# Performance work log

Measured on AMD Instinct MI355X. Metric: run time of the kernel, lower is better.

The kernel has to match this reference:

```python
import jax, jax.numpy as jnp
import numpy as np

N_STEPS = 8          # spatial_interval
SPATIAL_SCALE = 1.0  # spatial_scale


def setup_inputs() -> dict:
    key = jax.random.key(0)
    ks = jax.random.split(key, 6)
    B, N, D = 32, 1024, 256
    x = jax.random.normal(ks[0], (B, N, D), dtype=jnp.float32)
    adj_mx = jax.random.uniform(ks[1], (N, N), dtype=jnp.float32) / N  # row-scaled dense adjacency
    alpha_train = jnp.ones((N,), dtype=jnp.float32)          # alpha * ones(num_node), alpha=1.0
    w = jnp.eye(D, dtype=jnp.float32) + 0.01 * jax.random.normal(ks[2], (D, D), dtype=jnp.float32)
    d = jax.random.uniform(ks[3], (D,), dtype=jnp.float32)
    fc_in_w = jax.random.normal(ks[4], (D, D), dtype=jnp.float32) * (1.0 / np.sqrt(D))
    fc_in_b = jnp.zeros((D,), dtype=jnp.float32)
    return {"x": x, "adj_mx": adj_mx, "alpha_train": alpha_train, "w": w,
            "d": d, "fc_in_w": fc_in_w, "fc_in_b": fc_in_b, "vt": 0}


def reference(x, adj_mx, alpha_train, w, d, fc_in_w, fc_in_b, vt):
    # x: [B, N, D]. x0 is detached in torch (x.clone().detach()).
    x0 = jax.lax.stop_gradient(x)
    # fc_in (dropout is identity in eval mode)
    h = jnp.einsum('bnd,ed->bne', x, fc_in_w) + fc_in_b
    # constants of the diffusion ODE
    alph = jax.nn.sigmoid(alpha_train)[:, None]          # [N, 1]
    d_clamped = jnp.clip(d, 0.0, 1.0)
    w_eff = (w * d_clamped) @ w.T                        # [D, D]
    dt = jnp.float32(SPATIAL_SCALE / N_STEPS)

    def euler_step(h, _):
        ax = jnp.einsum('nm,bmd->bnd', adj_mx, h)        # graph diffusion
        f = alph * 0.5 * (ax - h) + h @ w_eff - h + x0
        return h + dt * f, None

    h, _ = jax.lax.scan(euler_step, h, None, length=N_STEPS)
    return h
```

## Files before the change

### kernel.cpp

```cpp
#include <hip/hip_runtime.h>
#include <hip/hip_bf16.h>
#include <stdint.h>

typedef __bf16 bf16;
typedef __bf16 bf16x8 __attribute__((ext_vector_type(8)));
typedef __bf16 bf16x4 __attribute__((ext_vector_type(4)));
typedef float f32x4 __attribute__((ext_vector_type(4)));

#define BM 128
#define BN 64
#define BK 64

__device__ __forceinline__ void gload_lds16(const bf16* g, bf16* l) {
    __builtin_amdgcn_global_load_lds(
        (const __attribute__((address_space(1))) void*)g,
        (__attribute__((address_space(3))) void*)l, 16, 0, 0);
}

template <int CH>
__device__ __forceinline__ void stageT(const bf16* __restrict__ g, int ld,
                                       bf16* l, int t) {
#pragma unroll
    for (int i = 0; i < CH / 256; ++i) {
        int c = (i << 8) + t;
        gload_lds16(g + (size_t)(c >> 3) * ld + ((c & 7) << 3), l + c * 8);
    }
}

__device__ __forceinline__ void mma_128x64(const bf16* As, const bf16* Bs,
                                           f32x4 acc[4][2], int lane, int wm, int wn) {
    const int rA = wm * 64 + (lane & 15);
    const int rB = wn * 32 + (lane & 15);
    const int kb = (lane >> 4) * 8;
#pragma unroll
    for (int kk = 0; kk < 2; ++kk) {
        bf16x8 a[4], b[2];
#pragma unroll
        for (int mi = 0; mi < 4; ++mi)
            a[mi] = *(const bf16x8*)&As[(rA + mi * 16) * BK + kk * 32 + kb];
#pragma unroll
        for (int ni = 0; ni < 2; ++ni)
            b[ni] = *(const bf16x8*)&Bs[(rB + ni * 16) * BK + kk * 32 + kb];
#pragma unroll
        for (int mi = 0; mi < 4; ++mi)
#pragma unroll
            for (int ni = 0; ni < 2; ++ni)
                acc[mi][ni] = __builtin_amdgcn_mfma_f32_16x16x32_bf16(
                    a[mi], b[ni], acc[mi][ni], 0, 0, 0);
    }
}

__global__ void prep_alpha(const float* __restrict__ a, float* __restrict__ out) {
    int i = blockIdx.x * blockDim.x + threadIdx.x;
    if (i < 1024) out[i] = 0.5f / (1.0f + __expf(-a[i]));
}

__global__ void prep_adj(const float* __restrict__ adj, const float* __restrict__ ahs,
                         bf16* __restrict__ adjb) {
    int i = blockIdx.x * blockDim.x + threadIdx.x;
    int row = i >> 8;
    float s = ahs[row];
    float4 v = ((const float4*)adj)[i];
    bf16x4 o = {(bf16)(s * v.x), (bf16)(s * v.y), (bf16)(s * v.z), (bf16)(s * v.w)};
    ((bf16x4*)adjb)[i] = o;
}

__global__ void cast_f32_bf16x4(const float* __restrict__ src, bf16* __restrict__ dst,
                                int n4) {
    int i = blockIdx.x * blockDim.x + threadIdx.x;
    if (i < n4) {
        float4 v = ((const float4*)src)[i];
        bf16x4 o = {(bf16)v.x, (bf16)v.y, (bf16)v.z, (bf16)v.w};
        ((bf16x4*)dst)[i] = o;
    }
}

__global__ void prep_weff(const float* __restrict__ w, const float* __restrict__ dv,
                          bf16* __restrict__ weffT) {
    __shared__ float wk[256];
    __shared__ float dd[256];
    int k = blockIdx.x, j = threadIdx.x;
    dd[j] = fminf(fmaxf(dv[j], 0.0f), 1.0f);
    wk[j] = w[k * 256 + j];
    __syncthreads();
    float s = 0.0f;
#pragma unroll 8
    for (int c = 0; c < 256; ++c) s += wk[c] * dd[c] * w[j * 256 + c];
    weffT[j * 256 + k] = (bf16)s;
}

__launch_bounds__(256)
__global__ void gemm_fcin(const bf16* __restrict__ xb, const bf16* __restrict__ fcwb,
                          const float* __restrict__ fcb, float* __restrict__ hf,
                          bf16* __restrict__ hb, bf16* __restrict__ hT) {
    __shared__ __align__(16) bf16 As[BM * BK];
    __shared__ __align__(16) bf16 Bs[BN * BK];
    int t = threadIdx.x, lane = t & 63, wv = t >> 6, wm = wv >> 1, wn = wv & 1;
    int row0 = blockIdx.y * BM;
    int col0 = blockIdx.x * BN;
    f32x4 acc[4][2] = {};
    const bf16* Ab = xb + (size_t)row0 * 256;
    const bf16* Bb = fcwb + (size_t)col0 * 256;
    for (int kt = 0; kt < 4; ++kt) {
        __syncthreads();
        stageT<1024>(Ab + kt * BK, 256, As, t);
        stageT<512>(Bb + kt * BK, 256, Bs, t);
        __syncthreads();
        mma_128x64(As, Bs, acc, lane, wm, wn);
    }
    int rbase = row0 + wm * 64 + ((lane >> 4) << 2);
    int cbase = col0 + wn * 32 + (lane & 15);
#pragma unroll
    for (int mi = 0; mi < 4; ++mi) {
        int rg = rbase + mi * 16;
#pragma unroll
        for (int ni = 0; ni < 2; ++ni) {
            int col = cbase + ni * 16;
            float bias = fcb[col];
            bf16x4 tv;
#pragma unroll
            for (int r = 0; r < 4; ++r) {
                float v = acc[mi][ni][r] + bias;
                size_t idx = (size_t)(rg + r) * 256 + col;
                hf[idx] = v;
                bf16 vb = (bf16)v;
                hb[idx] = vb;
                tv[r] = vb;
            }
            int b = rg >> 10, n = rg & 1023;
            *(bf16x4*)&hT[(((size_t)(b * 256 + col)) << 10) + n] = tv;
        }
    }
}

__launch_bounds__(256)
__global__ void gemm_step(const bf16* __restrict__ adjb, const bf16* __restrict__ hbp,
                          const bf16* __restrict__ hTp, const bf16* __restrict__ weffT,
                          const float* __restrict__ ahs, const bf16* __restrict__ x0b,
                          float* __restrict__ hf, bf16* __restrict__ hbn,
                          bf16* __restrict__ hTn) {
    __shared__ __align__(16) bf16 As[BM * BK];
    __shared__ __align__(16) bf16 Bs[BN * BK];
    int t = threadIdx.x, lane = t & 63, wv = t >> 6, wm = wv >> 1, wn = wv & 1;
    int g = blockIdx.x;
    int xcd = g & 7, rest = g >> 3;
    int xy = rest & 31, bhi = rest >> 5;
    int b = bhi * 8 + xcd;
    int d0 = (xy & 3) * BN;
    int n0 = (xy >> 2) * BM;
    f32x4 acc[4][2] = {};

    const bf16* Ab1 = adjb + (size_t)n0 * 1024;
    const bf16* Bb1 = hTp + ((size_t)(b * 256 + d0)) * 1024;
    for (int kt = 0; kt < 16; ++kt) {
        __syncthreads();
        stageT<1024>(Ab1 + kt * BK, 1024, As, t);
        stageT<512>(Bb1 + kt * BK, 1024, Bs, t);
        __syncthreads();
        mma_128x64(As, Bs, acc, lane, wm, wn);
    }
    const bf16* Ab2 = hbp + ((size_t)(b * 1024 + n0)) * 256;
    const bf16* Bb2 = weffT + (size_t)d0 * 256;
    for (int kt = 0; kt < 4; ++kt) {
        __syncthreads();
        stageT<1024>(Ab2 + kt * BK, 256, As, t);
        stageT<512>(Bb2 + kt * BK, 256, Bs, t);
        __syncthreads();
        mma_128x64(As, Bs, acc, lane, wm, wn);
    }

    const float dt = 0.125f;
    int rb = wm * 64 + ((lane >> 4) << 2);
    int cb = d0 + wn * 32 + (lane & 15);
#pragma unroll
    for (int mi = 0; mi < 4; ++mi) {
        int nr = n0 + rb + mi * 16;
#pragma unroll
        for (int ni = 0; ni < 2; ++ni) {
            int col = cb + ni * 16;
            bf16x4 tv;
#pragma unroll
            for (int r = 0; r < 4; ++r) {
                int node = nr + r;
                size_t idx = (((size_t)b << 10) + node) * 256 + col;
                float hold = hf[idx];
                float x0v = (float)x0b[idx];
                float f = acc[mi][ni][r] - (ahs[node] + 1.0f) * hold + x0v;
                float hv = hold + dt * f;
                hf[idx] = hv;
                bf16 vb = (bf16)hv;
                hbn[idx] = vb;
                tv[r] = vb;
            }
            *(bf16x4*)&hTn[(((size_t)(b * 256 + col)) << 10) + nr] = tv;
        }
    }
}

extern "C" void kernel_launch(void* const* d_in, const int* in_sizes, int n_in,
                              void* d_out, int out_size, void* d_ws, size_t ws_size,
                              hipStream_t stream) {
    const float* x     = (const float*)d_in[0];
    const float* adj   = (const float*)d_in[1];
    const float* alpha = (const float*)d_in[2];
    const float* w     = (const float*)d_in[3];
    const float* dvec  = (const float*)d_in[4];
    const float* fcw   = (const float*)d_in[5];
    const float* fcb   = (const float*)d_in[6];
    float* out = (float*)d_out;

    const size_t HB = (size_t)32 * 1024 * 256 * 2;
    char* p = (char*)d_ws;
    bf16* hb0   = (bf16*)p; p += HB;
    bf16* hb1   = (bf16*)p; p += HB;
    bf16* hT0   = (bf16*)p; p += HB;
    bf16* hT1   = (bf16*)p; p += HB;
    bf16* xb    = (bf16*)p; p += HB;
    bf16* adjb  = (bf16*)p; p += (size_t)1024 * 1024 * 2;
    bf16* fcwb  = (bf16*)p; p += 256 * 256 * 2;
    bf16* weffT = (bf16*)p; p += 256 * 256 * 2;
    float* ahs  = (float*)p; p += 1024 * 4;

    prep_alpha<<<4, 256, 0, stream>>>(alpha, ahs);
    prep_adj<<<1024, 256, 0, stream>>>(adj, ahs, adjb);
    prep_weff<<<256, 256, 0, stream>>>(w, dvec, weffT);
    cast_f32_bf16x4<<<8192, 256, 0, stream>>>(x, xb, 2097152);
    cast_f32_bf16x4<<<64, 256, 0, stream>>>(fcw, fcwb, 16384);

    gemm_fcin<<<dim3(4, 256), 256, 0, stream>>>(xb, fcwb, fcb, out, hb0, hT0);

    bf16* hb[2] = {hb0, hb1};
    bf16* hT[2] = {hT0, hT1};
    int cur = 0;
    for (int s = 0; s < 8; ++s) {
        gemm_step<<<1024, 256, 0, stream>>>(
            adjb, hb[cur], hT[cur], weffT, ahs, xb, out, hb[cur ^ 1], hT[cur ^ 1]);
        cur ^= 1;
    }
}
```

Baseline: 451.9 us.

## Load A fragments directly to registers, double-buffer swizzled B tiles in LDS

```diff
diff --git a/kernel.cpp b/kernel.cpp
--- a/kernel.cpp
+++ b/kernel.cpp
@@ -7,9 +7,6 @@
 typedef __bf16 bf16x4 __attribute__((ext_vector_type(4)));
 typedef float f32x4 __attribute__((ext_vector_type(4)));
 
-#define BM 128
-#define BN 64
-#define BK 64
 
 __device__ __forceinline__ void gload_lds16(const bf16* g, bf16* l) {
     __builtin_amdgcn_global_load_lds(
@@ -17,36 +14,72 @@
         (__attribute__((address_space(3))) void*)l, 16, 0, 0);
 }
 
-template <int CH>
-__device__ __forceinline__ void stageT(const bf16* __restrict__ g, int ld,
+__device__ __forceinline__ void stageB(const bf16* __restrict__ g, int ldb,
                                        bf16* l, int t) {
 #pragma unroll
-    for (int i = 0; i < CH / 256; ++i) {
+    for (int i = 0; i < 2; ++i) {
         int c = (i << 8) + t;
-        gload_lds16(g + (size_t)(c >> 3) * ld + ((c & 7) << 3), l + c * 8);
-    }
-}
-
-__device__ __forceinline__ void mma_128x64(const bf16* As, const bf16* Bs,
-                                           f32x4 acc[4][2], int lane, int wm, int wn) {
-    const int rA = wm * 64 + (lane & 15);
-    const int rB = wn * 32 + (lane & 15);
-    const int kb = (lane >> 4) * 8;
-#pragma unroll
-    for (int kk = 0; kk < 2; ++kk) {
-        bf16x8 a[4], b[2];
-#pragma unroll
-        for (int mi = 0; mi < 4; ++mi)
-            a[mi] = *(const bf16x8*)&As[(rA + mi * 16) * BK + kk * 32 + kb];
-#pragma unroll
-        for (int ni = 0; ni < 2; ++ni)
-            b[ni] = *(const bf16x8*)&Bs[(rB + ni * 16) * BK + kk * 32 + kb];
-#pragma unroll
-        for (int mi = 0; mi < 4; ++mi)
-#pragma unroll
-            for (int ni = 0; ni < 2; ++ni)
-                acc[mi][ni] = __builtin_amdgcn_mfma_f32_16x16x32_bf16(
-                    a[mi], b[ni], acc[mi][ni], 0, 0, 0);
+        int row = c >> 3, slot = c & 7;
+        gload_lds16(g + (size_t)row * ldb + ((slot ^ (row & 7)) << 3), l + c * 8);
+    }
+}
+
+template <int NKT>
+__device__ __forceinline__ void phase(const bf16* __restrict__ Ag, int lda,
+                                      const bf16* __restrict__ Bg, int ldb,
+                                      bf16* Bs, f32x4 acc[2][4], int t) {
+    const int lane = t & 63, wv = t >> 6;
+    const int arow = wv * 32 + (lane & 15);
+    const int acol = (lane >> 4) << 3;
+
+    bf16x8 aC[2][2], aN[2][2];
+#pragma unroll
+    for (int mi = 0; mi < 2; ++mi)
+#pragma unroll
+        for (int kk = 0; kk < 2; ++kk)
+            aC[mi][kk] = *(const bf16x8*)&Ag[(size_t)(arow + mi * 16) * lda +
+                                             kk * 32 + acol];
+    stageB(Bg, ldb, Bs, t);
+    __syncthreads();
+
+#pragma unroll
+    for (int kt = 0; kt < NKT; ++kt) {
+        const bf16* cur = Bs + (kt & 1) * 4096;
+        bf16* nxt = Bs + ((kt + 1) & 1) * 4096;
+        if (kt + 1 < NKT) {
+            stageB(Bg + (kt + 1) * 64, ldb, nxt, t);
+#pragma unroll
+            for (int mi = 0; mi < 2; ++mi)
+#pragma unroll
+                for (int kk = 0; kk < 2; ++kk)
+                    aN[mi][kk] = *(const bf16x8*)&Ag[(size_t)(arow + mi * 16) * lda +
+                                                     (kt + 1) * 64 + kk * 32 + acol];
+        }
+        bf16x8 b[4][2];
+#pragma unroll
+        for (int ni = 0; ni < 4; ++ni) {
+            int rB = ni * 16 + (lane & 15);
+#pragma unroll
+            for (int kk = 0; kk < 2; ++kk) {
+                int kc = kk * 4 + (lane >> 4);
+                b[ni][kk] = *(const bf16x8*)&cur[rB * 64 + ((kc ^ (rB & 7)) << 3)];
+            }
+        }
+#pragma unroll
+        for (int kk = 0; kk < 2; ++kk)
+#pragma unroll
+            for (int mi = 0; mi < 2; ++mi)
+#pragma unroll
+                for (int ni = 0; ni < 4; ++ni)
+                    acc[mi][ni] = __builtin_amdgcn_mfma_f32_16x16x32_bf16(
+                        aC[mi][kk], b[ni][kk], acc[mi][ni], 0, 0, 0);
+        if (kt + 1 < NKT) {
+#pragma unroll
+            for (int mi = 0; mi < 2; ++mi)
+#pragma unroll
+                for (int kk = 0; kk < 2; ++kk) aC[mi][kk] = aN[mi][kk];
+        }
+        __syncthreads();
     }
 }
 
@@ -89,32 +122,24 @@
     weffT[j * 256 + k] = (bf16)s;
 }
 
-__launch_bounds__(256)
+__launch_bounds__(256, 3)
 __global__ void gemm_fcin(const bf16* __restrict__ xb, const bf16* __restrict__ fcwb,
                           const float* __restrict__ fcb, float* __restrict__ hf,
                           bf16* __restrict__ hb, bf16* __restrict__ hT) {
-    __shared__ __align__(16) bf16 As[BM * BK];
-    __shared__ __align__(16) bf16 Bs[BN * BK];
-    int t = threadIdx.x, lane = t & 63, wv = t >> 6, wm = wv >> 1, wn = wv & 1;
-    int row0 = blockIdx.y * BM;
-    int col0 = blockIdx.x * BN;
-    f32x4 acc[4][2] = {};
-    const bf16* Ab = xb + (size_t)row0 * 256;
-    const bf16* Bb = fcwb + (size_t)col0 * 256;
-    for (int kt = 0; kt < 4; ++kt) {
-        __syncthreads();
-        stageT<1024>(Ab + kt * BK, 256, As, t);
-        stageT<512>(Bb + kt * BK, 256, Bs, t);
-        __syncthreads();
-        mma_128x64(As, Bs, acc, lane, wm, wn);
-    }
-    int rbase = row0 + wm * 64 + ((lane >> 4) << 2);
-    int cbase = col0 + wn * 32 + (lane & 15);
-#pragma unroll
-    for (int mi = 0; mi < 4; ++mi) {
+    __shared__ __align__(16) bf16 Bs[2 * 4096];
+    int t = threadIdx.x, lane = t & 63, wv = t >> 6;
+    int row0 = blockIdx.y * 128;
+    int col0 = blockIdx.x * 64;
+    f32x4 acc[2][4] = {};
+    phase<4>(xb + (size_t)row0 * 256, 256, fcwb + (size_t)col0 * 256, 256, Bs, acc, t);
+
+    int rbase = row0 + wv * 32 + ((lane >> 4) << 2);
+    int cbase = col0 + (lane & 15);
+#pragma unroll
+    for (int mi = 0; mi < 2; ++mi) {
         int rg = rbase + mi * 16;
 #pragma unroll
-        for (int ni = 0; ni < 2; ++ni) {
+        for (int ni = 0; ni < 4; ++ni) {
             int col = cbase + ni * 16;
             float bias = fcb[col];
             bf16x4 tv;
@@ -133,50 +158,35 @@
     }
 }
 
-__launch_bounds__(256)
+__launch_bounds__(256, 3)
 __global__ void gemm_step(const bf16* __restrict__ adjb, const bf16* __restrict__ hbp,
                           const bf16* __restrict__ hTp, const bf16* __restrict__ weffT,
                           const float* __restrict__ ahs, const bf16* __restrict__ x0b,
                           float* __restrict__ hf, bf16* __restrict__ hbn,
                           bf16* __restrict__ hTn) {
-    __shared__ __align__(16) bf16 As[BM * BK];
-    __shared__ __align__(16) bf16 Bs[BN * BK];
-    int t = threadIdx.x, lane = t & 63, wv = t >> 6, wm = wv >> 1, wn = wv & 1;
+    __shared__ __align__(16) bf16 Bs[2 * 4096];
+    int t = threadIdx.x, lane = t & 63, wv = t >> 6;
     int g = blockIdx.x;
     int xcd = g & 7, rest = g >> 3;
-    int xy = rest & 31, bhi = rest >> 5;
-    int b = bhi * 8 + xcd;
-    int d0 = (xy & 3) * BN;
-    int n0 = (xy >> 2) * BM;
-    f32x4 acc[4][2] = {};
-
-    const bf16* Ab1 = adjb + (size_t)n0 * 1024;
-    const bf16* Bb1 = hTp + ((size_t)(b * 256 + d0)) * 1024;
-    for (int kt = 0; kt < 16; ++kt) {
-        __syncthreads();
-        stageT<1024>(Ab1 + kt * BK, 1024, As, t);
-        stageT<512>(Bb1 + kt * BK, 1024, Bs, t);
-        __syncthreads();
-        mma_128x64(As, Bs, acc, lane, wm, wn);
-    }
-    const bf16* Ab2 = hbp + ((size_t)(b * 1024 + n0)) * 256;
-    const bf16* Bb2 = weffT + (size_t)d0 * 256;
-    for (int kt = 0; kt < 4; ++kt) {
-        __syncthreads();
-        stageT<1024>(Ab2 + kt * BK, 256, As, t);
-        stageT<512>(Bb2 + kt * BK, 256, Bs, t);
-        __syncthreads();
-        mma_128x64(As, Bs, acc, lane, wm, wn);
-    }
+    int xy = rest & 31;
+    int b = (rest >> 5) * 8 + xcd;
+    int d0 = (xy & 3) * 64;
+    int n0 = (xy >> 2) * 128;
+    f32x4 acc[2][4] = {};
+
+    phase<16>(adjb + (size_t)n0 * 1024, 1024,
+              hTp + ((size_t)(b * 256 + d0)) * 1024, 1024, Bs, acc, t);
+    phase<4>(hbp + ((size_t)(b * 1024 + n0)) * 256, 256,
+             weffT + (size_t)d0 * 256, 256, Bs, acc, t);
 
     const float dt = 0.125f;
-    int rb = wm * 64 + ((lane >> 4) << 2);
-    int cb = d0 + wn * 32 + (lane & 15);
-#pragma unroll
-    for (int mi = 0; mi < 4; ++mi) {
+    int rb = wv * 32 + ((lane >> 4) << 2);
+    int cb = d0 + (lane & 15);
+#pragma unroll
+    for (int mi = 0; mi < 2; ++mi) {
         int nr = n0 + rb + mi * 16;
 #pragma unroll
-        for (int ni = 0; ni < 2; ++ni) {
+        for (int ni = 0; ni < 4; ++ni) {
             int col = cb + ni * 16;
             bf16x4 tv;
 #pragma unroll
```

Result: slower. 516.1 us (+14.2%).
